# Performance work log

Measured on AMD Instinct MI355X. Metric: run time of the kernel, lower is better.

The kernel has to match this reference:

```python
import jax, jax.numpy as jnp
import numpy as np

EPS = 0.0  # init_eps=0, learn_eps=False -> fixed buffer
N_NODES = 50000
N_EDGES = 800000
D_NODE = 128
D_EDGE = 64


def setup_inputs() -> dict:
    key = jax.random.key(0)
    ks = jax.random.split(key, 10)
    s = lambda fan: 1.0 / np.sqrt(fan)
    return {
        "node_feat": jax.random.normal(ks[0], (N_NODES, D_NODE), jnp.float32),
        "edge_feat": jax.random.normal(ks[1], (N_EDGES, D_EDGE), jnp.float32),
        "W0": jax.random.normal(ks[2], (D_EDGE, D_EDGE), jnp.float32) * s(D_EDGE),
        "b0": jax.random.normal(ks[3], (D_EDGE,), jnp.float32) * s(D_EDGE),
        "W1": jax.random.normal(ks[4], (D_EDGE, D_NODE), jnp.float32) * s(D_EDGE),
        "b1": jax.random.normal(ks[5], (D_NODE,), jnp.float32) * s(D_EDGE),
        "Wa": jax.random.normal(ks[6], (D_NODE, D_NODE), jnp.float32) * s(D_NODE),
        "ba": jax.random.normal(ks[7], (D_NODE,), jnp.float32) * s(D_NODE),
        "src": jax.random.randint(ks[8], (N_EDGES,), 0, N_NODES, jnp.int64),
        "dst": jax.random.randint(ks[9], (N_EDGES,), 0, N_NODES, jnp.int64),
    }


def reference(node_feat, edge_feat, W0, b0, W1, b1, Wa, ba, src, dst):
    # edge transform MLP: relu(Linear) -> relu(Linear)  [E, D_NODE]
    e = jax.nn.relu(edge_feat @ W0 + b0)
    e = jax.nn.relu(e @ W1 + b1)
    # per-edge message: relu(x_src + e)  [E, D_NODE]
    m = jax.nn.relu(node_feat[src] + e)
    # scatter-sum to destination nodes  [N, D_NODE]
    neigh = jax.ops.segment_sum(m, dst, num_segments=node_feat.shape[0])
    rst = (1.0 + EPS) * node_feat + neigh
    # apply_func: Linear(128, 128)
    return rst @ Wa + ba
```

## Files before the change

### kernel.cpp

```cpp
#include <hip/hip_runtime.h>

typedef short bf16x8 __attribute__((ext_vector_type(8)));
typedef float f32x4 __attribute__((ext_vector_type(4)));
typedef unsigned short u16x2 __attribute__((ext_vector_type(2)));
typedef unsigned short u16x4 __attribute__((ext_vector_type(4)));
typedef unsigned short u16x8 __attribute__((ext_vector_type(8)));

static constexpr int N_NODES = 50000;
static constexpr int N_EDGES = 800000;
static constexpr int D_NODE = 128;
static constexpr int D_EDGE = 64;

static constexpr size_t START_OFF = 0;
static constexpr size_t FILL_OFF  = 262144;
static constexpr size_t META_OFF  = 524288;
static constexpr size_t NF16_OFF  = META_OFF + (size_t)N_EDGES * 16;
static constexpr size_t W0F_OFF   = NF16_OFF + (size_t)N_NODES * D_NODE * 2;
static constexpr size_t W1F_OFF   = W0F_OFF + 4096 * 2;
static constexpr size_t WS_NEED   = W1F_OFF + 8192 * 2;

__device__ __forceinline__ unsigned short f2bf(float f) {
    union { float f; unsigned u; } v; v.f = f;
    return (unsigned short)((v.u + 0x7fffu + ((v.u >> 16) & 1u)) >> 16);
}
__device__ __forceinline__ float bf2f(unsigned short h) {
    union { unsigned u; float f; } v; v.u = ((unsigned)h) << 16;
    return v.f;
}

__global__ void kz(int* __restrict__ a, int n) {
    int i = blockIdx.x * blockDim.x + threadIdx.x;
    if (i < n) a[i] = 0;
}

__global__ void kh(const int* __restrict__ dst, int* __restrict__ start) {
    int e = blockIdx.x * blockDim.x + threadIdx.x;
    if (e < N_EDGES) atomicAdd(&start[dst[e] + 1], 1);
}

__global__ __launch_bounds__(256) void ks1(const int* __restrict__ a, int* __restrict__ bsum, int n) {
    __shared__ int sd[256];
    const int t = threadIdx.x;
    int i = blockIdx.x * 256 + t;
    sd[t] = (i < n) ? a[i] : 0;
    __syncthreads();
    for (int off = 128; off > 0; off >>= 1) {
        if (t < off) sd[t] += sd[t + off];
        __syncthreads();
    }
    if (t == 0) bsum[blockIdx.x] = sd[0];
}

__global__ __launch_bounds__(256) void ks2(int* __restrict__ bsum, int nb) {
    __shared__ int sd[256];
    const int t = threadIdx.x;
    sd[t] = (t < nb) ? bsum[t] : 0;
    __syncthreads();
    for (int off = 1; off < 256; off <<= 1) {
        int v = (t >= off) ? sd[t - off] : 0;
        __syncthreads();
        sd[t] += v;
        __syncthreads();
    }
    if (t < nb) bsum[t] = sd[t];
}

__global__ __launch_bounds__(256) void ks3(const int* __restrict__ bsum,
                                           int* __restrict__ start, int* __restrict__ fill, int n) {
    __shared__ int sd[256];
    const int t = threadIdx.x;
    const int i = blockIdx.x * 256 + t;
    sd[t] = (i < n) ? start[i] : 0;
    __syncthreads();
    for (int off = 1; off < 256; off <<= 1) {
        int v = (t >= off) ? sd[t - off] : 0;
        __syncthreads();
        sd[t] += v;
        __syncthreads();
    }
    const int off0 = (blockIdx.x > 0) ? bsum[blockIdx.x - 1] : 0;
    const int val = sd[t] + off0;
    if (i < n) start[i] = val;
    if (i < N_NODES) fill[i] = val;
}

__global__ void kpos(const int* __restrict__ dst, const int* __restrict__ src,
                     int* __restrict__ fill, int4* __restrict__ meta) {
    int e = blockIdx.x * blockDim.x + threadIdx.x;
    if (e < N_EDGES) {
        int d = dst[e];
        int p = atomicAdd(&fill[d], 1);
        meta[p] = int4{e, src[e], d, 0};
    }
}

__global__ __launch_bounds__(256) void k_prep(const float* __restrict__ nf,
                                              float* __restrict__ out,
                                              unsigned short* __restrict__ nf16t) {
    const int tid = threadIdx.x;
    const int lm = tid & 15;
    const int node = blockIdx.x * 16 + (tid >> 4);
    if (node >= N_NODES) return;
    const float* nrow = nf + (size_t)node * D_NODE;
    float* orow = out + (size_t)node * D_NODE;
    f32x4 y0 = *(const f32x4*)(nrow + lm * 8);
    f32x4 y1 = *(const f32x4*)(nrow + lm * 8 + 4);
    *(f32x4*)(orow + lm * 8) = y0;
    *(f32x4*)(orow + lm * 8 + 4) = y1;
    u16x8 tv;
#pragma unroll
    for (int nt = 0; nt < 8; ++nt) tv[nt] = f2bf(nrow[nt * 16 + lm]);
    *(u16x8*)(nf16t + (size_t)node * D_NODE + lm * 8) = tv;
}

__global__ __launch_bounds__(256) void k_wprep(const float* __restrict__ W0,
                                               const float* __restrict__ W1,
                                               unsigned short* __restrict__ w0frag,
                                               unsigned short* __restrict__ w1frag) {
    const int f = blockIdx.x * 256 + threadIdx.x;
    if (f < 4096) {
        int j = f & 7, lane = (f >> 3) & 63, nt = (f >> 9) & 3, ks = (f >> 11) & 1;
        int k = ks * 32 + ((lane >> 4) << 2) + (j & 3) + ((j & 4) << 2);
        int n = nt * 16 + (lane & 15);
        w0frag[f] = f2bf(W0[k * 64 + n]);
    }
    if (f < 8192) {
        int j = f & 7, lane = (f >> 3) & 63, nt = (f >> 9) & 7, ks = (f >> 12) & 1;
        int k = ks * 32 + ((lane >> 4) << 2) + (j & 3) + ((j & 4) << 2);
        int n = nt * 16 + (lane & 15);
        w1frag[f] = f2bf(W1[k * 128 + n]);
    }
}

__global__ __launch_bounds__(256) void k_fused(
    const float* __restrict__ ef, const unsigned short* __restrict__ nf16t,
    const unsigned short* __restrict__ w0frag, const unsigned short* __restrict__ w1frag,
    const float* __restrict__ b0, const float* __restrict__ b1,
    const int4* __restrict__ meta, float* __restrict__ out)
{
    __shared__ __align__(16) unsigned short hT[4][16][72];
    __shared__ __align__(16) unsigned short mT[4][16][136];

    const int tid = threadIdx.x;

    int bid = blockIdx.x;
    {
        const int nwg = gridDim.x;
        const int q = nwg >> 3, rr = nwg & 7;
        const int xcd = bid & 7, j = bid >> 3;
        bid = (xcd < rr ? xcd * (q + 1) : rr * (q + 1) + (xcd - rr) * q) + j;
    }

    const int wv = tid >> 6;
    const int lane = tid & 63;
    const int lm = lane & 15;
    const int lq = lane >> 4;

    float b0r[4], b1r[8];
#pragma unroll
    for (int nt = 0; nt < 4; ++nt) b0r[nt] = b0[nt * 16 + lm];
#pragma unroll
    for (int nt = 0; nt < 8; ++nt) b1r[nt] = b1[nt * 16 + lm];

    const bf16x8* w0v = (const bf16x8*)w0frag;
    const bf16x8* w1v = (const bf16x8*)w1frag;

    const int wtile0 = (bid * 4 + wv) * 4;

    for (int t = 0; t < 4; ++t) {
        const int ebase = (wtile0 + t) * 16;

        const int4 m4 = meta[ebase + lm];
        const int e_m = m4.x, s_m = m4.y, d_m = m4.z;

        const f32x4* er = (const f32x4*)(ef + (size_t)e_m * D_EDGE);
        f32x4 a0 = er[lq];
        f32x4 a1 = er[4 + lq];
        f32x4 a2 = er[8 + lq];
        f32x4 a3 = er[12 + lq];

        u16x8 ngb[4];
#pragma unroll
        for (int r = 0; r < 4; ++r) {
            const int s_row = __shfl(s_m, lq * 4 + r);
            ngb[r] = *(const u16x8*)(nf16t + (size_t)s_row * D_NODE + lm * 8);
        }

        bf16x8 af0, af1;
#pragma unroll
        for (int j = 0; j < 4; ++j) {
            af0[j] = (short)f2bf(a0[j]); af0[j + 4] = (short)f2bf(a1[j]);
            af1[j] = (short)f2bf(a2[j]); af1[j + 4] = (short)f2bf(a3[j]);
        }

        f32x4 h[4];
#pragma unroll
        for (int nt = 0; nt < 4; ++nt) h[nt] = f32x4{0.f, 0.f, 0.f, 0.f};
#pragma unroll
        for (int nt = 0; nt < 4; ++nt) {
            h[nt] = __builtin_amdgcn_mfma_f32_16x16x32_bf16(af0, w0v[(0 * 4 + nt) * 64 + lane], h[nt], 0, 0, 0);
            h[nt] = __builtin_amdgcn_mfma_f32_16x16x32_bf16(af1, w0v[(1 * 4 + nt) * 64 + lane], h[nt], 0, 0, 0);
        }
#pragma unroll
        for (int nt = 0; nt < 4; ++nt)
#pragma unroll
            for (int r = 0; r < 4; ++r) {
                float x = h[nt][r] + b0r[nt];
                hT[wv][lq * 4 + r][nt * 16 + lm] = f2bf(fmaxf(x, 0.f));
            }

        const unsigned short* hrow = &hT[wv][lm][0];
        u16x4 p0 = *(const u16x4*)(hrow + lq * 4);
        u16x4 p1 = *(const u16x4*)(hrow + 16 + lq * 4);
        u16x4 p2 = *(const u16x4*)(hrow + 32 + lq * 4);
        u16x4 p3 = *(const u16x4*)(hrow + 48 + lq * 4);
        bf16x8 g0, g1;
#pragma unroll
        for (int j = 0; j < 4; ++j) {
            g0[j] = (short)p0[j]; g0[j + 4] = (short)p1[j];
            g1[j] = (short)p2[j]; g1[j + 4] = (short)p3[j];
        }

        f32x4 o[8];
#pragma unroll
        for (int nt = 0; nt < 8; ++nt) o[nt] = f32x4{0.f, 0.f, 0.f, 0.f};
#pragma unroll
        for (int nt = 0; nt < 8; ++nt) {
            o[nt] = __builtin_amdgcn_mfma_f32_16x16x32_bf16(g0, w1v[(0 * 8 + nt) * 64 + lane], o[nt], 0, 0, 0);
            o[nt] = __builtin_amdgcn_mfma_f32_16x16x32_bf16(g1, w1v[(1 * 8 + nt) * 64 + lane], o[nt], 0, 0, 0);
        }

#pragma unroll
        for (int nt = 0; nt < 8; ++nt)
#pragma unroll
            for (int r = 0; r < 4; ++r) {
                float e2 = fmaxf(o[nt][r] + b1r[nt], 0.f);
                float x = e2 + bf2f(ngb[r][nt]);
                mT[wv][lq * 4 + r][nt * 16 + lm] = f2bf(fmaxf(x, 0.f));
            }

        asm volatile("s_waitcnt lgkmcnt(0)" ::: "memory");
        __builtin_amdgcn_sched_barrier(0);

        float acc0 = 0.f, acc1 = 0.f;
        int dprev = __shfl(d_m, 0);
#pragma unroll
        for (int r = 0; r < 16; ++r) {
            const int dr = __shfl(d_m, r);
            if (dr != dprev) {
                float* orow = out + (size_t)dprev * D_NODE + lane * 2;
                unsafeAtomicAdd(orow, acc0);
                unsafeAtomicAdd(orow + 1, acc1);
                acc0 = 0.f; acc1 = 0.f; dprev = dr;
            }
            const u16x2 v = *(const u16x2*)&mT[wv][r][lane * 2];
            acc0 += bf2f(v[0]);
            acc1 += bf2f(v[1]);
        }
        float* orow = out + (size_t)dprev * D_NODE + lane * 2;
        unsafeAtomicAdd(orow, acc0);
        unsafeAtomicAdd(orow + 1, acc1);

        asm volatile("" ::: "memory");
    }
}

__global__ void k_copy(const f32x4* __restrict__ s, f32x4* __restrict__ d, int n4) {
    int stride = gridDim.x * blockDim.x;
    for (int i = blockIdx.x * blockDim.x + threadIdx.x; i < n4; i += stride)
        d[i] = s[i];
}

__global__ __launch_bounds__(256) void k_edge(
    const float* __restrict__ ef, const float* __restrict__ nf,
    const float* __restrict__ W0, const float* __restrict__ b0,
    const float* __restrict__ W1, const float* __restrict__ b1,
    const int* __restrict__ src, const int* __restrict__ dst,
    float* __restrict__ acc)
{
    __shared__ unsigned short w0f[2 * 4 * 64 * 8];
    __shared__ unsigned short w1f[2 * 8 * 64 * 8];
    __shared__ unsigned short hT[4][16][72];

    const int tid = threadIdx.x;
    for (int f = tid; f < 4096; f += 256) {
        int j = f & 7, lane = (f >> 3) & 63, nt = (f >> 9) & 3, ks = (f >> 11) & 1;
        int k = ks * 32 + ((lane >> 4) << 2) + (j & 3) + ((j & 4) << 2);
        int n = nt * 16 + (lane & 15);
        w0f[f] = f2bf(W0[k * 64 + n]);
    }
    for (int f = tid; f < 8192; f += 256) {
        int j = f & 7, lane = (f >> 3) & 63, nt = (f >> 9) & 7, ks = (f >> 12) & 1;
        int k = ks * 32 + ((lane >> 4) << 2) + (j & 3) + ((j & 4) << 2);
        int n = nt * 16 + (lane & 15);
        w1f[f] = f2bf(W1[k * 128 + n]);
    }
    __syncthreads();

    const int wv = tid >> 6;
    const int lane = tid & 63;
    const int lm = lane & 15;
    const int lq = lane >> 4;

    float b0r[4], b1r[8];
#pragma unroll
    for (int nt = 0; nt < 4; ++nt) b0r[nt] = b0[nt * 16 + lm];
#pragma unroll
    for (int nt = 0; nt < 8; ++nt) b1r[nt] = b1[nt * 16 + lm];

    const bf16x8* w0v = (const bf16x8*)w0f;
    const bf16x8* w1v = (const bf16x8*)w1f;

    for (int t = 0; t < 4; ++t) {
        const int tile = (blockIdx.x * 4 + wv) * 4 + t;
        const int ebase = tile * 16;

        const f32x4* er = (const f32x4*)(ef + (size_t)(ebase + lm) * D_EDGE);
        f32x4 a0 = er[lq];
        f32x4 a1 = er[4 + lq];
        f32x4 a2 = er[8 + lq];
        f32x4 a3 = er[12 + lq];
        bf16x8 af0, af1;
#pragma unroll
        for (int j = 0; j < 4; ++j) {
            af0[j] = (short)f2bf(a0[j]); af0[j + 4] = (short)f2bf(a1[j]);
            af1[j] = (short)f2bf(a2[j]); af1[j + 4] = (short)f2bf(a3[j]);
        }

        f32x4 h[4];
#pragma unroll
        for (int nt = 0; nt < 4; ++nt) h[nt] = f32x4{0.f, 0.f, 0.f, 0.f};
#pragma unroll
        for (int nt = 0; nt < 4; ++nt) {
            h[nt] = __builtin_amdgcn_mfma_f32_16x16x32_bf16(af0, w0v[(0 * 4 + nt) * 64 + lane], h[nt], 0, 0, 0);
            h[nt] = __builtin_amdgcn_mfma_f32_16x16x32_bf16(af1, w0v[(1 * 4 + nt) * 64 + lane], h[nt], 0, 0, 0);
        }
#pragma unroll
        for (int nt = 0; nt < 4; ++nt)
#pragma unroll
            for (int r = 0; r < 4; ++r) {
                float x = h[nt][r] + b0r[nt];
                hT[wv][lq * 4 + r][nt * 16 + lm] = f2bf(fmaxf(x, 0.f));
            }

        const unsigned short* hrow = &hT[wv][lm][0];
        u16x4 p0 = *(const u16x4*)(hrow + lq * 4);
        u16x4 p1 = *(const u16x4*)(hrow + 16 + lq * 4);
        u16x4 p2 = *(const u16x4*)(hrow + 32 + lq * 4);
        u16x4 p3 = *(const u16x4*)(hrow + 48 + lq * 4);
        bf16x8 g0, g1;
#pragma unroll
        for (int j = 0; j < 4; ++j) {
            g0[j] = (short)p0[j]; g0[j + 4] = (short)p1[j];
            g1[j] = (short)p2[j]; g1[j + 4] = (short)p3[j];
        }

        f32x4 o[8];
#pragma unroll
        for (int nt = 0; nt < 8; ++nt) o[nt] = f32x4{0.f, 0.f, 0.f, 0.f};
#pragma unroll
        for (int nt = 0; nt < 8; ++nt) {
            o[nt] = __builtin_amdgcn_mfma_f32_16x16x32_bf16(g0, w1v[(0 * 8 + nt) * 64 + lane], o[nt], 0, 0, 0);
            o[nt] = __builtin_amdgcn_mfma_f32_16x16x32_bf16(g1, w1v[(1 * 8 + nt) * 64 + lane], o[nt], 0, 0, 0);
        }

        const int e0 = ebase + lq * 4;
        int s_[4], d_[4];
#pragma unroll
        for (int r = 0; r < 4; ++r) { s_[r] = src[e0 + r]; d_[r] = dst[e0 + r]; }
#pragma unroll
        for (int r = 0; r < 4; ++r) {
            const float* nrow = nf + (size_t)s_[r] * D_NODE;
            float* arow = acc + (size_t)d_[r] * D_NODE;
#pragma unroll
            for (int nt = 0; nt < 8; ++nt) {
                float e2 = fmaxf(o[nt][r] + b1r[nt], 0.f);
                float x = e2 + nrow[nt * 16 + lm];
                unsafeAtomicAdd(&arow[nt * 16 + lm], fmaxf(x, 0.f));
            }
        }
    }
}

__global__ __launch_bounds__(256) void k_out(
    const float* __restrict__ Wa, const float* __restrict__ ba,
    float* __restrict__ out)
{
    __shared__ unsigned short waf[4 * 8 * 64 * 8];

    const int tid = threadIdx.x;
    for (int f = tid; f < 16384; f += 256) {
        int j = f & 7, lane = (f >> 3) & 63, nt = (f >> 9) & 7, ks = (f >> 12) & 3;
        int k = ks * 32 + ((lane >> 4) << 2) + (j & 3) + ((j & 4) << 2);
        int n = nt * 16 + (lane & 15);
        waf[f] = f2bf(Wa[k * 128 + n]);
    }
    __syncthreads();

    const int wv = tid >> 6;
    const int lane = tid & 63;
    const int lm = lane & 15;
    const int lq = lane >> 4;

    const int tile = blockIdx.x * 4 + wv;
    if (tile >= N_NODES / 16) return;
    const int rbase = tile * 16;

    const f32x4* arow = (const f32x4*)(out + (size_t)(rbase + lm) * D_NODE);
    const bf16x8* wav = (const bf16x8*)waf;

    bf16x8 afr[4];
#pragma unroll
    for (int ks = 0; ks < 4; ++ks) {
        f32x4 y0 = arow[ks * 8 + lq];
        f32x4 y1 = arow[ks * 8 + 4 + lq];
#pragma unroll
        for (int j = 0; j < 4; ++j) {
            afr[ks][j] = (short)f2bf(y0[j]);
            afr[ks][j + 4] = (short)f2bf(y1[j]);
        }
    }

    float bar[8];
#pragma unroll
    for (int nt = 0; nt < 8; ++nt) bar[nt] = ba[nt * 16 + lm];

    f32x4 o[8];
#pragma unroll
    for (int nt = 0; nt < 8; ++nt) o[nt] = f32x4{0.f, 0.f, 0.f, 0.f};
#pragma unroll
    for (int ks = 0; ks < 4; ++ks)
#pragma unroll
        for (int nt = 0; nt < 8; ++nt)
            o[nt] = __builtin_amdgcn_mfma_f32_16x16x32_bf16(afr[ks], wav[(ks * 8 + nt) * 64 + lane], o[nt], 0, 0, 0);

#pragma unroll
    for (int nt = 0; nt < 8; ++nt)
#pragma unroll
        for (int r = 0; r < 4; ++r)
            out[(size_t)(rbase + lq * 4 + r) * D_NODE + nt * 16 + lm] = o[nt][r] + bar[nt];
}

extern "C" void kernel_launch(void* const* d_in, const int* in_sizes, int n_in,
                              void* d_out, int out_size, void* d_ws, size_t ws_size,
                              hipStream_t stream) {
    const float* nf = (const float*)d_in[0];
    const float* ef = (const float*)d_in[1];
    const float* W0 = (const float*)d_in[2];
    const float* b0 = (const float*)d_in[3];
    const float* W1 = (const float*)d_in[4];
    const float* b1 = (const float*)d_in[5];
    const float* Wa = (const float*)d_in[6];
    const float* ba = (const float*)d_in[7];
    const int* src = (const int*)d_in[8];
    const int* dst = (const int*)d_in[9];
    float* out = (float*)d_out;

    if (ws_size >= WS_NEED) {
        char* ws = (char*)d_ws;
        int* start = (int*)(ws + START_OFF);
        int* fill  = (int*)(ws + FILL_OFF);
        int4* meta = (int4*)(ws + META_OFF);
        unsigned short* nf16t = (unsigned short*)(ws + NF16_OFF);
        unsigned short* w0frag = (unsigned short*)(ws + W0F_OFF);
        unsigned short* w1frag = (unsigned short*)(ws + W1F_OFF);
        int* bsum  = (int*)(ws + META_OFF);

        const int n_scan = N_NODES + 1;
        const int nb = (n_scan + 255) / 256;

        k_prep<<<(N_NODES + 15) / 16, 256, 0, stream>>>(nf, out, nf16t);
        k_wprep<<<32, 256, 0, stream>>>(W0, W1, w0frag, w1frag);

        kz<<<(n_scan + 255) / 256, 256, 0, stream>>>(start, n_scan);
        kh<<<(N_EDGES + 255) / 256, 256, 0, stream>>>(dst, start);
        ks1<<<nb, 256, 0, stream>>>(start, bsum, n_scan);
        ks2<<<1, 256, 0, stream>>>(bsum, nb);
        ks3<<<nb, 256, 0, stream>>>(bsum, start, fill, n_scan);
        kpos<<<(N_EDGES + 255) / 256, 256, 0, stream>>>(dst, src, fill, meta);

        k_fused<<<N_EDGES / 256, 256, 0, stream>>>(
            ef, nf16t, w0frag, w1frag, b0, b1, meta, out);
    } else {
        k_copy<<<2048, 256, 0, stream>>>((const f32x4*)nf, (f32x4*)out, N_NODES * D_NODE / 4);
        k_edge<<<N_EDGES / (16 * 4 * 4), 256, 0, stream>>>(ef, nf, W0, b0, W1, b1, src, dst, out);
    }

    k_out<<<(N_NODES / 16 + 3) / 4, 256, 0, stream>>>(Wa, ba, out);
}
```

Measured before the change: 264.9 us.

## Reduce segments in registers via shuffles and merge prep launches

The per-edge segment reduction in the fused kernel now runs in registers from the MFMA output layout, using cross-quad xor shuffles, instead of staging bf16 messages through a shared-memory tile. This removes the LDS round trip and its wait. The weight-fragment prep kernel is folded into the node prep kernel as extra blocks, and the zeroing kernel is replaced by hipMemsetAsync, which cuts launch count. In exchange, every destination change inside a 16-edge group now costs 16 shuffles, which may hurt when consecutive edges go to different nodes.

```diff
diff --git a/kernel.cpp b/kernel.cpp
--- a/kernel.cpp
+++ b/kernel.cpp
@@ -26,11 +26,6 @@
 __device__ __forceinline__ float bf2f(unsigned short h) {
     union { unsigned u; float f; } v; v.u = ((unsigned)h) << 16;
     return v.f;
-}
-
-__global__ void kz(int* __restrict__ a, int n) {
-    int i = blockIdx.x * blockDim.x + threadIdx.x;
-    if (i < n) a[i] = 0;
 }
 
 __global__ void kh(const int* __restrict__ dst, int* __restrict__ start) {
@@ -96,7 +91,28 @@
 
 __global__ __launch_bounds__(256) void k_prep(const float* __restrict__ nf,
                                               float* __restrict__ out,
-                                              unsigned short* __restrict__ nf16t) {
+                                              unsigned short* __restrict__ nf16t,
+                                              const float* __restrict__ W0,
+                                              const float* __restrict__ W1,
+                                              unsigned short* __restrict__ w0frag,
+                                              unsigned short* __restrict__ w1frag,
+                                              int nprep) {
+    if ((int)blockIdx.x >= nprep) {
+        const int f = ((int)blockIdx.x - nprep) * 256 + threadIdx.x;
+        if (f < 4096) {
+            int j = f & 7, lane = (f >> 3) & 63, nt = (f >> 9) & 3, ks = (f >> 11) & 1;
+            int k = ks * 32 + ((lane >> 4) << 2) + (j & 3) + ((j & 4) << 2);
+            int n = nt * 16 + (lane & 15);
+            w0frag[f] = f2bf(W0[k * 64 + n]);
+        }
+        if (f < 8192) {
+            int j = f & 7, lane = (f >> 3) & 63, nt = (f >> 9) & 7, ks = (f >> 12) & 1;
+            int k = ks * 32 + ((lane >> 4) << 2) + (j & 3) + ((j & 4) << 2);
+            int n = nt * 16 + (lane & 15);
+            w1frag[f] = f2bf(W1[k * 128 + n]);
+        }
+        return;
+    }
     const int tid = threadIdx.x;
     const int lm = tid & 15;
     const int node = blockIdx.x * 16 + (tid >> 4);
@@ -113,25 +129,6 @@
     *(u16x8*)(nf16t + (size_t)node * D_NODE + lm * 8) = tv;
 }
 
-__global__ __launch_bounds__(256) void k_wprep(const float* __restrict__ W0,
-                                               const float* __restrict__ W1,
-                                               unsigned short* __restrict__ w0frag,
-                                               unsigned short* __restrict__ w1frag) {
-    const int f = blockIdx.x * 256 + threadIdx.x;
-    if (f < 4096) {
-        int j = f & 7, lane = (f >> 3) & 63, nt = (f >> 9) & 3, ks = (f >> 11) & 1;
-        int k = ks * 32 + ((lane >> 4) << 2) + (j & 3) + ((j & 4) << 2);
-        int n = nt * 16 + (lane & 15);
-        w0frag[f] = f2bf(W0[k * 64 + n]);
-    }
-    if (f < 8192) {
-        int j = f & 7, lane = (f >> 3) & 63, nt = (f >> 9) & 7, ks = (f >> 12) & 1;
-        int k = ks * 32 + ((lane >> 4) << 2) + (j & 3) + ((j & 4) << 2);
-        int n = nt * 16 + (lane & 15);
-        w1frag[f] = f2bf(W1[k * 128 + n]);
-    }
-}
-
 __global__ __launch_bounds__(256) void k_fused(
     const float* __restrict__ ef, const unsigned short* __restrict__ nf16t,
     const unsigned short* __restrict__ w0frag, const unsigned short* __restrict__ w1frag,
@@ -139,7 +136,6 @@
     const int4* __restrict__ meta, float* __restrict__ out)
 {
     __shared__ __align__(16) unsigned short hT[4][16][72];
-    __shared__ __align__(16) unsigned short mT[4][16][136];
 
     const int tid = threadIdx.x;
 
@@ -235,33 +231,50 @@
 #pragma unroll
             for (int r = 0; r < 4; ++r) {
                 float e2 = fmaxf(o[nt][r] + b1r[nt], 0.f);
-                float x = e2 + bf2f(ngb[r][nt]);
-                mT[wv][lq * 4 + r][nt * 16 + lm] = f2bf(fmaxf(x, 0.f));
-            }
-
-        asm volatile("s_waitcnt lgkmcnt(0)" ::: "memory");
-        __builtin_amdgcn_sched_barrier(0);
-
-        float acc0 = 0.f, acc1 = 0.f;
-        int dprev = __shfl(d_m, 0);
-#pragma unroll
-        for (int r = 0; r < 16; ++r) {
-            const int dr = __shfl(d_m, r);
-            if (dr != dprev) {
-                float* orow = out + (size_t)dprev * D_NODE + lane * 2;
-                unsafeAtomicAdd(orow, acc0);
-                unsafeAtomicAdd(orow + 1, acc1);
-                acc0 = 0.f; acc1 = 0.f; dprev = dr;
-            }
-            const u16x2 v = *(const u16x2*)&mT[wv][r][lane * 2];
-            acc0 += bf2f(v[0]);
-            acc1 += bf2f(v[1]);
-        }
-        float* orow = out + (size_t)dprev * D_NODE + lane * 2;
-        unsafeAtomicAdd(orow, acc0);
-        unsafeAtomicAdd(orow + 1, acc1);
-
-        asm volatile("" ::: "memory");
+                float x = fmaxf(e2 + bf2f(ngb[r][nt]), 0.f);
+                o[nt][r] = bf2f(f2bf(x));
+            }
+
+        float acc[8];
+#pragma unroll
+        for (int nt = 0; nt < 8; ++nt) acc[nt] = 0.f;
+        int dcur = __builtin_amdgcn_readlane(d_m, 0);
+
+#pragma unroll
+        for (int i = 0; i < 16; ++i) {
+            const int di = __builtin_amdgcn_readlane(d_m, i);
+            if (di != dcur) {
+#pragma unroll
+                for (int nt = 0; nt < 8; ++nt) {
+                    acc[nt] += __shfl_xor(acc[nt], 16);
+                    acc[nt] += __shfl_xor(acc[nt], 32);
+                }
+                float v0 = (lq & 2) ? ((lq & 1) ? acc[6] : acc[4]) : ((lq & 1) ? acc[2] : acc[0]);
+                float v1 = (lq & 2) ? ((lq & 1) ? acc[7] : acc[5]) : ((lq & 1) ? acc[3] : acc[1]);
+                float* orow = out + (size_t)dcur * D_NODE + lq * 32 + lm;
+                unsafeAtomicAdd(orow, v0);
+                unsafeAtomicAdd(orow + 16, v1);
+#pragma unroll
+                for (int nt = 0; nt < 8; ++nt) acc[nt] = 0.f;
+                dcur = di;
+            }
+            if (lq == (i >> 2)) {
+#pragma unroll
+                for (int nt = 0; nt < 8; ++nt) acc[nt] += o[nt][i & 3];
+            }
+        }
+        {
+#pragma unroll
+            for (int nt = 0; nt < 8; ++nt) {
+                acc[nt] += __shfl_xor(acc[nt], 16);
+                acc[nt] += __shfl_xor(acc[nt], 32);
+            }
+            float v0 = (lq & 2) ? ((lq & 1) ? acc[6] : acc[4]) : ((lq & 1) ? acc[2] : acc[0]);
+            float v1 = (lq & 2) ? ((lq & 1) ? acc[7] : acc[5]) : ((lq & 1) ? acc[3] : acc[1]);
+            float* orow = out + (size_t)dcur * D_NODE + lq * 32 + lm;
+            unsafeAtomicAdd(orow, v0);
+            unsafeAtomicAdd(orow + 16, v1);
+        }
     }
 }
 
@@ -468,11 +481,12 @@
 
         const int n_scan = N_NODES + 1;
         const int nb = (n_scan + 255) / 256;
-
-        k_prep<<<(N_NODES + 15) / 16, 256, 0, stream>>>(nf, out, nf16t);
-        k_wprep<<<32, 256, 0, stream>>>(W0, W1, w0frag, w1frag);
-
-        kz<<<(n_scan + 255) / 256, 256, 0, stream>>>(start, n_scan);
+        const int nprep = (N_NODES + 15) / 16;
+
+        hipMemsetAsync(start, 0, n_scan * sizeof(int), stream);
+
+        k_prep<<<nprep + 32, 256, 0, stream>>>(nf, out, nf16t, W0, W1, w0frag, w1frag, nprep);
+
         kh<<<(N_EDGES + 255) / 256, 256, 0, stream>>>(dst, start);
         ks1<<<nb, 256, 0, stream>>>(start, bsum, n_scan);
         ks2<<<1, 256, 0, stream>>>(bsum, nb);
```

New measurement: 272.6 us. +2.9%, slower.
